# Kernel tuning notes

Measured on AMD Instinct MI355X. Metric: run time of the kernel, lower is better.

The kernel has to match this reference:

```python
import jax, jax.numpy as jnp
import numpy as np

B, N, C, F, E, K = 2, 2048, 1024, 4096, 8, 2

def setup_inputs() -> dict:
    key = jax.random.key(0)
    k = jax.random.split(key, 6)
    xavier1 = float(np.sqrt(6.0 / (C + F)))
    xavier2 = float(np.sqrt(6.0 / (F + C)))
    return {
        "x": jax.random.normal(k[0], (B, N, C), dtype=jnp.float32),
        "router_w": jax.random.normal(k[1], (E, C), dtype=jnp.float32) * 0.01,
        "w1": jax.random.uniform(k[2], (E, F, C), dtype=jnp.float32, minval=-xavier1, maxval=xavier1),
        "b1": jnp.zeros((E, F), dtype=jnp.float32),
        "w2": jax.random.uniform(k[3], (E, C, F), dtype=jnp.float32, minval=-xavier2, maxval=xavier2),
        "b2": jnp.zeros((E, C), dtype=jnp.float32),
    }

def reference(x, router_w, w1, b1, w2, b2):
    Bb, Nn, Cc = x.shape
    x_flat = x.reshape(-1, Cc)                                   # [T, C]
    # Router (eval mode: no noise)
    logits = jnp.einsum('tc,ec->te', x_flat, router_w)           # [T, E]
    probs = jax.nn.softmax(logits, axis=-1)
    top_w, top_idx = jax.lax.top_k(probs, K)                     # [T, K]
    top_w = top_w / (jnp.sum(top_w, axis=-1, keepdims=True) + 1e-9)
    # Dense all-expert MLP (same math as the per-expert gather/scatter loop)
    h = jnp.einsum('tc,efc->tef', x_flat, w1) + b1[None]          # [T, E, F]
    h = jax.nn.relu(h)
    y = jnp.einsum('tef,ecf->tec', h, w2) + b2[None]              # [T, E, C]
    # Gather the K selected experts per token and combine
    sel = jnp.take_along_axis(y, top_idx[:, :, None], axis=1)    # [T, K, C]
    out = jnp.einsum('tkc,tk->tc', sel, top_w)                   # [T, C]
    return out.reshape(Bb, Nn, Cc)
```

## Files before the change

### kernel.cpp

```cpp
#include <hip/hip_runtime.h>
#include <hip/hip_fp16.h>


#define T_TOK 4096
#define C_DIM 1024
#define F_DIM 4096
#define E_NUM 8
#define BM 128
#define BN 128
#define BK 64
#define MAXT 72
#define TILE_H 8192

typedef float f32x4 __attribute__((ext_vector_type(4)));
typedef _Float16 half8 __attribute__((ext_vector_type(8)));

#define AS1 __attribute__((address_space(1)))
#define AS3 __attribute__((address_space(3)))

__device__ __forceinline__ int swz(int r, int ec) { return ec ^ ((r & 7) << 3); }

__device__ __forceinline__ half8 cvt8(float4 f0, float4 f1) {
  half8 hv;
  hv[0] = (_Float16)f0.x; hv[1] = (_Float16)f0.y; hv[2] = (_Float16)f0.z; hv[3] = (_Float16)f0.w;
  hv[4] = (_Float16)f1.x; hv[5] = (_Float16)f1.y; hv[6] = (_Float16)f1.z; hv[7] = (_Float16)f1.w;
  return hv;
}

__global__ __launch_bounds__(256) void router_kernel(
    const float* __restrict__ x, const float* __restrict__ rw,
    int* __restrict__ top_idx, float* __restrict__ top_w)
{
  int t = blockIdx.x * 4 + (threadIdx.x >> 6);
  int lane = threadIdx.x & 63;
  const float* xr = x + (size_t)t * C_DIM;
  float acc[E_NUM];
#pragma unroll
  for (int e = 0; e < E_NUM; ++e) acc[e] = 0.f;
  for (int j = 0; j < C_DIM / 64; ++j) {
    int c = j * 64 + lane;
    float xv = xr[c];
#pragma unroll
    for (int e = 0; e < E_NUM; ++e) acc[e] += xv * rw[e * C_DIM + c];
  }
#pragma unroll
  for (int e = 0; e < E_NUM; ++e) {
    float v = acc[e];
#pragma unroll
    for (int off = 32; off > 0; off >>= 1) v += __shfl_xor(v, off);
    acc[e] = v;
  }
  if (lane == 0) {
    float mx = acc[0];
    for (int e = 1; e < E_NUM; ++e) mx = fmaxf(mx, acc[e]);
    float p[E_NUM]; float Z = 0.f;
    for (int e = 0; e < E_NUM; ++e) { p[e] = expf(acc[e] - mx); Z += p[e]; }
    int b0 = 0;
    for (int e = 1; e < E_NUM; ++e) if (p[e] > p[b0]) b0 = e;
    int b1i = -1; float pb = -1.f;
    for (int e = 0; e < E_NUM; ++e) if (e != b0 && p[e] > pb) { pb = p[e]; b1i = e; }
    float p0 = p[b0] / Z, p1 = pb / Z;
    float s = p0 + p1 + 1e-9f;
    top_idx[t * 2 + 0] = b0;
    top_idx[t * 2 + 1] = b1i;
    top_w[t * 2 + 0] = p0 / s;
    top_w[t * 2 + 1] = p1 / s;
  }
}

__global__ void build_lists(const int* __restrict__ top_idx,
                            int* __restrict__ rows_g, int* __restrict__ counts,
                            int* __restrict__ tile_off)
{
  int e = threadIdx.x >> 6;
  int lane = threadIdx.x & 63;
  int cnt = 0;
  for (int t0 = 0; t0 < T_TOK; t0 += 64) {
    int t = t0 + lane;
    bool sel = (top_idx[t * 2] == e) || (top_idx[t * 2 + 1] == e);
    cnt += __popcll(__ballot(sel));
  }
  if (lane == 0) counts[e] = cnt;
  __syncthreads();
  if (threadIdx.x == 0) {
    int o = 0;
    for (int i = 0; i < E_NUM; ++i) { tile_off[i] = o; o += (counts[i] + BM - 1) / BM; }
    tile_off[E_NUM] = o;
  }
  __syncthreads();
  int base = tile_off[e] * BM;
  int pos = 0;
  for (int t0 = 0; t0 < T_TOK; t0 += 64) {
    int t = t0 + lane;
    int i0 = top_idx[t * 2], i1 = top_idx[t * 2 + 1];
    bool sel = (i0 == e) || (i1 == e);
    unsigned long long mask = __ballot(sel);
    if (sel) {
      int p = pos + __popcll(mask & ((1ull << lane) - 1ull));
      rows_g[base + p] = t * 2 + ((i0 == e) ? 0 : 1);
    }
    pos += __popcll(mask);
  }
}

__global__ __launch_bounds__(256) void gather_x(
    const float* __restrict__ x, const int* __restrict__ rows_g,
    const int* __restrict__ counts, const int* __restrict__ tile_off,
    _Float16* __restrict__ xg)
{
  unsigned g = blockIdx.x * 256 + threadIdx.x;
  unsigned p = g >> 7, ccr = g & 127;
  int gt = p >> 7, r = p & 127;
  int kc = ccr >> 3, c8 = ccr & 7;
  int e = -1;
#pragma unroll
  for (int i = 0; i < E_NUM; ++i)
    if (gt >= tile_off[i] && gt < tile_off[i + 1]) e = i;
  half8 hv = {};
  if (e >= 0) {
    int nrem = counts[e] - (gt - tile_off[e]) * BM;
    if (r < nrem) {
      int t = rows_g[p] >> 1;
      const float4* s = reinterpret_cast<const float4*>(x + (size_t)t * C_DIM + kc * 64 + c8 * 8);
      hv = cvt8(s[0], s[1]);
    }
  }
  *reinterpret_cast<half8*>(xg + ((size_t)gt * 16 + kc) * TILE_H + r * 64 + ((c8 ^ (r & 7)) << 3)) = hv;
}

__global__ __launch_bounds__(256) void cvt_w1(
    const float* __restrict__ src, _Float16* __restrict__ dst, int ch, int Fc, int lgFc)
{
  unsigned g = blockIdx.x * 256 + threadIdx.x;
  unsigned row = g >> 7, ccr = g & 127;
  int e = row >> lgFc, frow = row & (Fc - 1);
  int ftl = frow >> 7, r = frow & 127;
  int kc = ccr >> 3, c8 = ccr & 7;
  const float4* s = reinterpret_cast<const float4*>(
      src + ((size_t)e * F_DIM + ch * Fc + frow) * C_DIM + kc * 64 + c8 * 8);
  int nft = Fc >> 7;
  size_t tix = ((size_t)(e * nft + ftl) * 16 + kc);
  *reinterpret_cast<half8*>(dst + tix * TILE_H + r * 64 + ((c8 ^ (r & 7)) << 3)) = cvt8(s[0], s[1]);
}

__global__ __launch_bounds__(256) void cvt_w2(
    const float* __restrict__ src, _Float16* __restrict__ dst, int ch, int Fc, int lgc)
{
  unsigned g = blockIdx.x * 256 + threadIdx.x;
  unsigned row = g >> lgc, ccr = g & ((Fc >> 3) - 1);
  int e = row >> 10, c = row & 1023;
  int ct = c >> 7, r = c & 127;
  int kc = ccr >> 3, c8 = ccr & 7;
  const float4* s = reinterpret_cast<const float4*>(
      src + (size_t)row * F_DIM + ch * Fc + kc * 64 + c8 * 8);
  int nkc = Fc >> 6;
  size_t tix = ((size_t)(e * 8 + ct) * nkc + kc);
  *reinterpret_cast<half8*>(dst + tix * TILE_H + r * 64 + ((c8 ^ (r & 7)) << 3)) = cvt8(s[0], s[1]);
}

__global__ __launch_bounds__(256) void gemm1_kernel(
    const _Float16* __restrict__ xg, const _Float16* __restrict__ w1t,
    const float* __restrict__ b1, const int* __restrict__ counts,
    const int* __restrict__ tile_off, _Float16* __restrict__ ht,
    int ch, int Fc)
{
  const int gt = blockIdx.x;
  if (gt >= tile_off[E_NUM]) return;
  int e = 0;
  while (gt >= tile_off[e + 1]) ++e;
  const int nrem = min(counts[e] - (gt - tile_off[e]) * BM, BM);
  const int ft = blockIdx.y;
  const int nft = Fc >> 7;
  const _Float16* At = xg + (size_t)gt * 16 * TILE_H;
  const _Float16* Bt = w1t + (size_t)(e * nft + ft) * 16 * TILE_H;

  __shared__ __align__(16) _Float16 As[TILE_H];
  __shared__ __align__(16) _Float16 Bs[TILE_H];

  const int tid = threadIdx.x;
  const int lane = tid & 63;
  const int wave = tid >> 6;
  const int wr = wave >> 1, wc = wave & 1;

  f32x4 acc[4][4];
#pragma unroll
  for (int m = 0; m < 4; ++m)
#pragma unroll
    for (int n = 0; n < 4; ++n) acc[m][n] = (f32x4){0.f, 0.f, 0.f, 0.f};

  for (int kc = 0; kc < 16; ++kc) {
    const _Float16* a = At + kc * TILE_H + wave * 2048 + lane * 8;
    const _Float16* b = Bt + kc * TILE_H + wave * 2048 + lane * 8;
#pragma unroll
    for (int c = 0; c < 4; ++c) {
      __builtin_amdgcn_global_load_lds((const AS1 void*)(a + c * 512),
                                       (AS3 void*)(As + (wave * 4 + c) * 512), 16, 0, 0);
      __builtin_amdgcn_global_load_lds((const AS1 void*)(b + c * 512),
                                       (AS3 void*)(Bs + (wave * 4 + c) * 512), 16, 0, 0);
    }
    __syncthreads();
#pragma unroll
    for (int kk = 0; kk < BK; kk += 32) {
      const int klo = kk + (lane >> 4) * 8;
      half8 aF[4], bF[4];
#pragma unroll
      for (int m = 0; m < 4; ++m) {
        int r = wr * 64 + m * 16 + (lane & 15);
        aF[m] = *reinterpret_cast<const half8*>(&As[r * BK + swz(r, klo)]);
      }
#pragma unroll
      for (int n = 0; n < 4; ++n) {
        int r = wc * 64 + n * 16 + (lane & 15);
        bF[n] = *reinterpret_cast<const half8*>(&Bs[r * BK + swz(r, klo)]);
      }
#pragma unroll
      for (int m = 0; m < 4; ++m)
#pragma unroll
        for (int n = 0; n < 4; ++n)
          acc[m][n] = __builtin_amdgcn_mfma_f32_16x16x32_f16(aF[m], bF[n], acc[m][n], 0, 0, 0);
    }
    __syncthreads();
  }

  const int nkcF = Fc >> 6;
#pragma unroll
  for (int m = 0; m < 4; ++m) {
#pragma unroll
    for (int j = 0; j < 4; ++j) {
      int iloc = wr * 64 + m * 16 + (lane >> 4) * 4 + j;
      if (iloc < nrem) {
#pragma unroll
        for (int n = 0; n < 4; ++n) {
          int fl = ft * BN + wc * 64 + n * 16 + (lane & 15);
          float v = acc[m][n][j] + b1[e * F_DIM + ch * Fc + fl];
          _Float16 h = (_Float16)fmaxf(v, 0.f);
          ht[((size_t)gt * nkcF + (fl >> 6)) * TILE_H + iloc * 64 +
             ((((fl >> 3) & 7) ^ (iloc & 7)) << 3) + (fl & 7)] = h;
        }
      }
    }
  }
}

__global__ __launch_bounds__(256) void gemm2_kernel(
    const _Float16* __restrict__ ht, const _Float16* __restrict__ w2t,
    const float* __restrict__ b2, const int* __restrict__ rows_g,
    const int* __restrict__ counts, const int* __restrict__ tile_off,
    const float* __restrict__ top_w, float* __restrict__ out,
    int Fc, int kspl, int add_bias)
{
  const int gt = blockIdx.x;
  if (gt >= tile_off[E_NUM]) return;
  int e = 0;
  while (gt >= tile_off[e + 1]) ++e;
  const int nrem = min(counts[e] - (gt - tile_off[e]) * BM, BM);
  const int ct = blockIdx.y & 7;
  const int ks = blockIdx.y >> 3;
  const int nkc = Fc >> 6;
  const int klen = nkc / kspl;
  const _Float16* At = ht + (size_t)gt * nkc * TILE_H;
  const _Float16* Bt = w2t + (size_t)(e * 8 + ct) * nkc * TILE_H;

  __shared__ __align__(16) _Float16 As[TILE_H];
  __shared__ __align__(16) _Float16 Bs[TILE_H];

  const int tid = threadIdx.x;
  const int lane = tid & 63;
  const int wave = tid >> 6;
  const int wr = wave >> 1, wc = wave & 1;

  f32x4 acc[4][4];
#pragma unroll
  for (int m = 0; m < 4; ++m)
#pragma unroll
    for (int n = 0; n < 4; ++n) acc[m][n] = (f32x4){0.f, 0.f, 0.f, 0.f};

  for (int kc = ks * klen; kc < (ks + 1) * klen; ++kc) {
    const _Float16* a = At + (size_t)kc * TILE_H + wave * 2048 + lane * 8;
    const _Float16* b = Bt + (size_t)kc * TILE_H + wave * 2048 + lane * 8;
#pragma unroll
    for (int c = 0; c < 4; ++c) {
      __builtin_amdgcn_global_load_lds((const AS1 void*)(a + c * 512),
                                       (AS3 void*)(As + (wave * 4 + c) * 512), 16, 0, 0);
      __builtin_amdgcn_global_load_lds((const AS1 void*)(b + c * 512),
                                       (AS3 void*)(Bs + (wave * 4 + c) * 512), 16, 0, 0);
    }
    __syncthreads();
#pragma unroll
    for (int kk = 0; kk < BK; kk += 32) {
      const int klo = kk + (lane >> 4) * 8;
      half8 aF[4], bF[4];
#pragma unroll
      for (int m = 0; m < 4; ++m) {
        int r = wr * 64 + m * 16 + (lane & 15);
        aF[m] = *reinterpret_cast<const half8*>(&As[r * BK + swz(r, klo)]);
      }
#pragma unroll
      for (int n = 0; n < 4; ++n) {
        int r = wc * 64 + n * 16 + (lane & 15);
        bF[n] = *reinterpret_cast<const half8*>(&Bs[r * BK + swz(r, klo)]);
      }
#pragma unroll
      for (int m = 0; m < 4; ++m)
#pragma unroll
        for (int n = 0; n < 4; ++n)
          acc[m][n] = __builtin_amdgcn_mfma_f32_16x16x32_f16(aF[m], bF[n], acc[m][n], 0, 0, 0);
    }
    __syncthreads();
  }

#pragma unroll
  for (int m = 0; m < 4; ++m) {
#pragma unroll
    for (int j = 0; j < 4; ++j) {
      int iloc = wr * 64 + m * 16 + (lane >> 4) * 4 + j;
      if (iloc < nrem) {
        int slot = rows_g[gt * BM + iloc];
        int t = slot >> 1;
        float wgt = top_w[slot];
#pragma unroll
        for (int n = 0; n < 4; ++n) {
          int c = ct * BN + wc * 64 + n * 16 + (lane & 15);
          float v = acc[m][n][j];
          if (add_bias && ks == 0) v += b2[e * C_DIM + c];
          atomicAdd(out + (size_t)t * C_DIM + c, wgt * v);
        }
      }
    }
  }
}

extern "C" void kernel_launch(void* const* d_in, const int* in_sizes, int n_in,
                              void* d_out, int out_size, void* d_ws, size_t ws_size,
                              hipStream_t stream)
{
  const float* x  = (const float*)d_in[0];
  const float* rw = (const float*)d_in[1];
  const float* w1 = (const float*)d_in[2];
  const float* b1 = (const float*)d_in[3];
  const float* w2 = (const float*)d_in[4];
  const float* b2 = (const float*)d_in[5];
  float* out = (float*)d_out;

  char* ws = (char*)d_ws;
  size_t off = 0;
  auto carve = [&](size_t bytes) -> void* {
    void* p = ws + off;
    off += (bytes + 255) & ~(size_t)255;
    return p;
  };
  int*   top_idx  = (int*)carve((size_t)T_TOK * 2 * sizeof(int));
  float* top_w    = (float*)carve((size_t)T_TOK * 2 * sizeof(float));
  int*   counts   = (int*)carve(E_NUM * sizeof(int));
  int*   tile_off = (int*)carve((E_NUM + 1) * sizeof(int));
  int*   rows_g   = (int*)carve((size_t)MAXT * BM * sizeof(int));
  _Float16* xg    = (_Float16*)carve((size_t)MAXT * 16 * TILE_H * sizeof(_Float16));
  size_t fixed = off;

  int nchunk = 8;
  const int cands[4] = {1, 2, 4, 8};
  for (int ci = 0; ci < 4; ++ci) {
    int n = cands[ci];
    size_t fc = (size_t)(F_DIM / n);
    size_t w1b = ((size_t)E_NUM * fc * C_DIM * 2 + 255) & ~(size_t)255;
    size_t w2b = ((size_t)E_NUM * C_DIM * fc * 2 + 255) & ~(size_t)255;
    size_t htb = ((size_t)MAXT * (fc >> 6) * TILE_H * 2 + 255) & ~(size_t)255;
    if (fixed + w1b + w2b + htb <= ws_size) { nchunk = n; break; }
  }
  const int Fc = F_DIM / nchunk;
  int lgFc = 0; while ((1 << lgFc) < Fc) ++lgFc;
  _Float16* w1t = (_Float16*)carve((size_t)E_NUM * Fc * C_DIM * sizeof(_Float16));
  _Float16* w2t = (_Float16*)carve((size_t)E_NUM * C_DIM * Fc * sizeof(_Float16));
  _Float16* ht  = (_Float16*)carve((size_t)MAXT * (Fc >> 6) * TILE_H * sizeof(_Float16));

  const int kspl = (Fc >= 2048) ? 2 : 1;

  hipMemsetAsync(out, 0, (size_t)out_size * sizeof(float), stream);
  router_kernel<<<T_TOK / 4, 256, 0, stream>>>(x, rw, top_idx, top_w);
  build_lists<<<1, 512, 0, stream>>>(top_idx, rows_g, counts, tile_off);
  gather_x<<<(MAXT * BM * 128) / 256, 256, 0, stream>>>(x, rows_g, counts, tile_off, xg);

  const int cvt_blocks = 4 * Fc;
  for (int ch = 0; ch < nchunk; ++ch) {
    cvt_w1<<<cvt_blocks, 256, 0, stream>>>(w1, w1t, ch, Fc, lgFc);
    cvt_w2<<<cvt_blocks, 256, 0, stream>>>(w2, w2t, ch, Fc, lgFc - 3);
    gemm1_kernel<<<dim3(MAXT, Fc / BN), 256, 0, stream>>>(
        xg, w1t, b1, counts, tile_off, ht, ch, Fc);
    gemm2_kernel<<<dim3(MAXT, 8 * kspl), 256, 0, stream>>>(
        ht, w2t, b2, rows_g, counts, tile_off, top_w, out, Fc, kspl, ch == 0);
  }
}
```

Before: 419.9 us.

## Double-buffer LDS tiles in expert GEMMs and remap workgroups across XCDs

Both expert GEMM kernels now use two LDS buffers and issue the global-to-LDS loads for the next K tile before computing the current one, waiting with explicit vmcnt counts and raw s_barrier calls. The goal is to hide global load latency behind the MFMA work. The 2D grid is also flattened to 1D, and block IDs are remapped so that consecutive logical workgroups land on the same XCD, which should improve L2 reuse of the shared weight and activation tiles. The cost is twice the LDS per block, which may lower occupancy, and hand-tuned waitcnt values that are fragile.

```diff
diff --git a/kernel.cpp b/kernel.cpp
--- a/kernel.cpp
+++ b/kernel.cpp
@@ -25,6 +25,12 @@
   hv[0] = (_Float16)f0.x; hv[1] = (_Float16)f0.y; hv[2] = (_Float16)f0.z; hv[3] = (_Float16)f0.w;
   hv[4] = (_Float16)f1.x; hv[5] = (_Float16)f1.y; hv[6] = (_Float16)f1.z; hv[7] = (_Float16)f1.w;
   return hv;
+}
+
+__device__ __forceinline__ int xcd_swz(int bid, int nwg) {
+  int xcd = bid & 7, rest = bid >> 3;
+  int q = nwg >> 3, r = nwg & 7;
+  return (xcd < r ? xcd * (q + 1) : r * (q + 1) + (xcd - r) * q) + rest;
 }
 
 __global__ __launch_bounds__(256) void router_kernel(
@@ -158,24 +164,60 @@
   *reinterpret_cast<half8*>(dst + tix * TILE_H + r * 64 + ((c8 ^ (r & 7)) << 3)) = cvt8(s[0], s[1]);
 }
 
+#define STAGE_TILE(At_, Bt_, kc_, buf_)                                           \
+  {                                                                               \
+    const _Float16* a_ = (At_) + (size_t)(kc_) * TILE_H + wave * 2048 + lane * 8; \
+    const _Float16* b_ = (Bt_) + (size_t)(kc_) * TILE_H + wave * 2048 + lane * 8; \
+    _Pragma("unroll")                                                             \
+    for (int c_ = 0; c_ < 4; ++c_) {                                              \
+      __builtin_amdgcn_global_load_lds((const AS1 void*)(a_ + c_ * 512),          \
+          (AS3 void*)(&As[buf_][(wave * 4 + c_) * 512]), 16, 0, 0);               \
+      __builtin_amdgcn_global_load_lds((const AS1 void*)(b_ + c_ * 512),          \
+          (AS3 void*)(&Bs[buf_][(wave * 4 + c_) * 512]), 16, 0, 0);               \
+    }                                                                             \
+  }
+
+#define COMPUTE_TILE(buf_)                                                        \
+  _Pragma("unroll")                                                               \
+  for (int kk = 0; kk < BK; kk += 32) {                                           \
+    const int klo = kk + (lane >> 4) * 8;                                         \
+    half8 aF[4], bF[4];                                                           \
+    _Pragma("unroll")                                                             \
+    for (int m = 0; m < 4; ++m) {                                                 \
+      int r = wr * 64 + m * 16 + (lane & 15);                                     \
+      aF[m] = *reinterpret_cast<const half8*>(&As[buf_][r * BK + swz(r, klo)]);   \
+    }                                                                             \
+    _Pragma("unroll")                                                             \
+    for (int n = 0; n < 4; ++n) {                                                 \
+      int r = wc * 64 + n * 16 + (lane & 15);                                     \
+      bF[n] = *reinterpret_cast<const half8*>(&Bs[buf_][r * BK + swz(r, klo)]);   \
+    }                                                                             \
+    _Pragma("unroll")                                                             \
+    for (int m = 0; m < 4; ++m)                                                   \
+      _Pragma("unroll")                                                           \
+      for (int n = 0; n < 4; ++n)                                                 \
+        acc[m][n] = __builtin_amdgcn_mfma_f32_16x16x32_f16(aF[m], bF[n], acc[m][n], 0, 0, 0); \
+  }
+
 __global__ __launch_bounds__(256) void gemm1_kernel(
     const _Float16* __restrict__ xg, const _Float16* __restrict__ w1t,
     const float* __restrict__ b1, const int* __restrict__ counts,
     const int* __restrict__ tile_off, _Float16* __restrict__ ht,
     int ch, int Fc)
 {
-  const int gt = blockIdx.x;
+  const int wgid = xcd_swz(blockIdx.x, gridDim.x);
+  const int ft = wgid / MAXT;
+  const int gt = wgid - ft * MAXT;
   if (gt >= tile_off[E_NUM]) return;
   int e = 0;
   while (gt >= tile_off[e + 1]) ++e;
   const int nrem = min(counts[e] - (gt - tile_off[e]) * BM, BM);
-  const int ft = blockIdx.y;
   const int nft = Fc >> 7;
   const _Float16* At = xg + (size_t)gt * 16 * TILE_H;
   const _Float16* Bt = w1t + (size_t)(e * nft + ft) * 16 * TILE_H;
 
-  __shared__ __align__(16) _Float16 As[TILE_H];
-  __shared__ __align__(16) _Float16 Bs[TILE_H];
+  __shared__ __align__(16) _Float16 As[2][TILE_H];
+  __shared__ __align__(16) _Float16 Bs[2][TILE_H];
 
   const int tid = threadIdx.x;
   const int lane = tid & 63;
@@ -188,38 +230,22 @@
 #pragma unroll
     for (int n = 0; n < 4; ++n) acc[m][n] = (f32x4){0.f, 0.f, 0.f, 0.f};
 
+  STAGE_TILE(At, Bt, 0, 0);
+  int cur = 0;
   for (int kc = 0; kc < 16; ++kc) {
-    const _Float16* a = At + kc * TILE_H + wave * 2048 + lane * 8;
-    const _Float16* b = Bt + kc * TILE_H + wave * 2048 + lane * 8;
-#pragma unroll
-    for (int c = 0; c < 4; ++c) {
-      __builtin_amdgcn_global_load_lds((const AS1 void*)(a + c * 512),
-                                       (AS3 void*)(As + (wave * 4 + c) * 512), 16, 0, 0);
-      __builtin_amdgcn_global_load_lds((const AS1 void*)(b + c * 512),
-                                       (AS3 void*)(Bs + (wave * 4 + c) * 512), 16, 0, 0);
-    }
-    __syncthreads();
-#pragma unroll
-    for (int kk = 0; kk < BK; kk += 32) {
-      const int klo = kk + (lane >> 4) * 8;
-      half8 aF[4], bF[4];
-#pragma unroll
-      for (int m = 0; m < 4; ++m) {
-        int r = wr * 64 + m * 16 + (lane & 15);
-        aF[m] = *reinterpret_cast<const half8*>(&As[r * BK + swz(r, klo)]);
-      }
-#pragma unroll
-      for (int n = 0; n < 4; ++n) {
-        int r = wc * 64 + n * 16 + (lane & 15);
-        bF[n] = *reinterpret_cast<const half8*>(&Bs[r * BK + swz(r, klo)]);
-      }
-#pragma unroll
-      for (int m = 0; m < 4; ++m)
-#pragma unroll
-        for (int n = 0; n < 4; ++n)
-          acc[m][n] = __builtin_amdgcn_mfma_f32_16x16x32_f16(aF[m], bF[n], acc[m][n], 0, 0, 0);
-    }
-    __syncthreads();
+    if (kc + 1 < 16) {
+      STAGE_TILE(At, Bt, kc + 1, cur ^ 1);
+      asm volatile("s_waitcnt vmcnt(8)" ::: "memory");
+    } else {
+      asm volatile("s_waitcnt vmcnt(0)" ::: "memory");
+    }
+    __builtin_amdgcn_sched_barrier(0);
+    __builtin_amdgcn_s_barrier();
+    __builtin_amdgcn_sched_barrier(0);
+    COMPUTE_TILE(cur);
+    __builtin_amdgcn_sched_barrier(0);
+    __builtin_amdgcn_s_barrier();
+    cur ^= 1;
   }
 
   const int nkcF = Fc >> 6;
@@ -249,20 +275,22 @@
     const float* __restrict__ top_w, float* __restrict__ out,
     int Fc, int kspl, int add_bias)
 {
-  const int gt = blockIdx.x;
+  const int wgid = xcd_swz(blockIdx.x, gridDim.x);
+  const int ctks = wgid / MAXT;
+  const int gt = wgid - ctks * MAXT;
   if (gt >= tile_off[E_NUM]) return;
+  const int ct = ctks & 7;
+  const int ks = ctks >> 3;
   int e = 0;
   while (gt >= tile_off[e + 1]) ++e;
   const int nrem = min(counts[e] - (gt - tile_off[e]) * BM, BM);
-  const int ct = blockIdx.y & 7;
-  const int ks = blockIdx.y >> 3;
   const int nkc = Fc >> 6;
   const int klen = nkc / kspl;
-  const _Float16* At = ht + (size_t)gt * nkc * TILE_H;
-  const _Float16* Bt = w2t + (size_t)(e * 8 + ct) * nkc * TILE_H;
-
-  __shared__ __align__(16) _Float16 As[TILE_H];
-  __shared__ __align__(16) _Float16 Bs[TILE_H];
+  const _Float16* At = ht + ((size_t)gt * nkc + ks * klen) * TILE_H;
+  const _Float16* Bt = w2t + ((size_t)(e * 8 + ct) * nkc + ks * klen) * TILE_H;
+
+  __shared__ __align__(16) _Float16 As[2][TILE_H];
+  __shared__ __align__(16) _Float16 Bs[2][TILE_H];
 
   const int tid = threadIdx.x;
   const int lane = tid & 63;
@@ -275,38 +303,22 @@
 #pragma unroll
     for (int n = 0; n < 4; ++n) acc[m][n] = (f32x4){0.f, 0.f, 0.f, 0.f};
 
-  for (int kc = ks * klen; kc < (ks + 1) * klen; ++kc) {
-    const _Float16* a = At + (size_t)kc * TILE_H + wave * 2048 + lane * 8;
-    const _Float16* b = Bt + (size_t)kc * TILE_H + wave * 2048 + lane * 8;
-#pragma unroll
-    for (int c = 0; c < 4; ++c) {
-      __builtin_amdgcn_global_load_lds((const AS1 void*)(a + c * 512),
-                                       (AS3 void*)(As + (wave * 4 + c) * 512), 16, 0, 0);
-      __builtin_amdgcn_global_load_lds((const AS1 void*)(b + c * 512),
-                                       (AS3 void*)(Bs + (wave * 4 + c) * 512), 16, 0, 0);
-    }
-    __syncthreads();
-#pragma unroll
-    for (int kk = 0; kk < BK; kk += 32) {
-      const int klo = kk + (lane >> 4) * 8;
-      half8 aF[4], bF[4];
-#pragma unroll
-      for (int m = 0; m < 4; ++m) {
-        int r = wr * 64 + m * 16 + (lane & 15);
-        aF[m] = *reinterpret_cast<const half8*>(&As[r * BK + swz(r, klo)]);
-      }
-#pragma unroll
-      for (int n = 0; n < 4; ++n) {
-        int r = wc * 64 + n * 16 + (lane & 15);
-        bF[n] = *reinterpret_cast<const half8*>(&Bs[r * BK + swz(r, klo)]);
-      }
-#pragma unroll
-      for (int m = 0; m < 4; ++m)
-#pragma unroll
-        for (int n = 0; n < 4; ++n)
-          acc[m][n] = __builtin_amdgcn_mfma_f32_16x16x32_f16(aF[m], bF[n], acc[m][n], 0, 0, 0);
-    }
-    __syncthreads();
+  STAGE_TILE(At, Bt, 0, 0);
+  int cur = 0;
+  for (int kc = 0; kc < klen; ++kc) {
+    if (kc + 1 < klen) {
+      STAGE_TILE(At, Bt, kc + 1, cur ^ 1);
+      asm volatile("s_waitcnt vmcnt(8)" ::: "memory");
+    } else {
+      asm volatile("s_waitcnt vmcnt(0)" ::: "memory");
+    }
+    __builtin_amdgcn_sched_barrier(0);
+    __builtin_amdgcn_s_barrier();
+    __builtin_amdgcn_sched_barrier(0);
+    COMPUTE_TILE(cur);
+    __builtin_amdgcn_sched_barrier(0);
+    __builtin_amdgcn_s_barrier();
+    cur ^= 1;
   }
 
 #pragma unroll
@@ -384,9 +396,9 @@
   for (int ch = 0; ch < nchunk; ++ch) {
     cvt_w1<<<cvt_blocks, 256, 0, stream>>>(w1, w1t, ch, Fc, lgFc);
     cvt_w2<<<cvt_blocks, 256, 0, stream>>>(w2, w2t, ch, Fc, lgFc - 3);
-    gemm1_kernel<<<dim3(MAXT, Fc / BN), 256, 0, stream>>>(
+    gemm1_kernel<<<MAXT * (Fc / BN), 256, 0, stream>>>(
         xg, w1t, b1, counts, tile_off, ht, ch, Fc);
-    gemm2_kernel<<<dim3(MAXT, 8 * kspl), 256, 0, stream>>>(
+    gemm2_kernel<<<MAXT * 8 * kspl, 256, 0, stream>>>(
         ht, w2t, b2, rows_g, counts, tile_off, top_w, out, Fc, kspl, ch == 0);
   }
 }
```

New measurement: 474.1 us. 12.9% more time.
